# Optimization experiments

Measured on AMD Instinct MI355X. Metric: run time of the kernel, lower is better.

The kernel has to match this reference:

```python
import jax, jax.numpy as jnp
import numpy as np

NUM_EXPS = [8, 16, 64, 256, 1024]
KS = [4, 4, 32, 32, 256]
HIDDEN = 256
OUT_DIM = 3
IN_DIM = 2
N_IMGS = 2
N_COORDS = 1024


def setup_inputs() -> dict:
    key = jax.random.key(0)
    ks = jax.random.split(key, 16)
    inp = {}
    inp["raw_gates"] = jax.random.normal(ks[0], (N_IMGS, sum(NUM_EXPS)), jnp.float32)
    inp["coords"] = jax.random.uniform(ks[1], (N_COORDS, IN_DIM), jnp.float32, -1.0, 1.0)
    fan_in = [IN_DIM] + [HIDDEN] * 4
    fan_out = [HIDDEN * e for e in NUM_EXPS[:-1]] + [OUT_DIM * NUM_EXPS[-1]]
    for i, (fi, fo) in enumerate(zip(fan_in, fan_out)):
        # first_layer_sine_init / sine_init weight scales from the torch module
        bound = (1.0 / fi) if i == 0 else (np.sqrt(6.0 / fi) / 30.0)
        inp[f"W{i}"] = jax.random.uniform(ks[2 + 2 * i], (fo, fi), jnp.float32, -bound, bound)
        bb = 1.0 / np.sqrt(fi)  # torch nn.Linear default bias init
        inp[f"b{i}"] = jax.random.uniform(ks[3 + 2 * i], (fo,), jnp.float32, -bb, bb)
    return inp


def _topk_gate(g, k):
    # torch: topk(|g|, k+1) -> keep top k, gather signed values, scatter into zeros
    _, idx = jax.lax.top_k(jnp.abs(g), min(k + 1, g.shape[1]))
    idx = idx[:, :k]
    vals = jnp.take_along_axis(g, idx, axis=1)
    rows = jnp.arange(g.shape[0])[:, None]
    return jnp.zeros_like(g).at[rows, idx].set(vals)


def _forward(raw_gates, coords, Ws, bs):
    offs = np.cumsum([0] + NUM_EXPS)
    gates = [_topk_gate(raw_gates[:, offs[i]:offs[i + 1]], KS[i]) for i in range(len(NUM_EXPS))]
    Ni = raw_gates.shape[0]
    Nc = coords.shape[0]
    E0 = NUM_EXPS[0]
    # layer 0: shared experts, combine = sparse gates @ expert outputs (== MoECombiner scatter-add)
    h = jnp.sin(30.0 * (coords @ Ws[0].T + bs[0]))            # [Nc, H*E0]
    h = h.reshape(Nc, HIDDEN, E0).transpose(2, 0, 1).reshape(E0, Nc * HIDDEN)  # [E0, Nc*H]
    x = (gates[0] @ h).reshape(Ni, Nc, HIDDEN)                # [Ni, Nc, H]
    for i in range(1, len(NUM_EXPS)):
        E = NUM_EXPS[i]
        h = x @ Ws[i].T + bs[i]                               # [Ni, Nc, d*E]
        if i < len(NUM_EXPS) - 1:
            h = jnp.sin(30.0 * h)
            d = HIDDEN
        else:
            d = OUT_DIM                                       # last layer: no activation
        h = h.reshape(Ni, Nc, d, E)
        x = jnp.einsum('icde,ie->icd', h, gates[i])           # bmm(gate, experts)
    return x


def reference(raw_gates, coords, W0, b0, W1, b1, W2, b2, W3, b3, W4, b4):
    return _forward(raw_gates, coords, (W0, W1, W2, W3, W4), (b0, b1, b2, b3, b4))
```

## Files before the change

### kernel.cpp

```cpp
#include <hip/hip_runtime.h>
#include <math.h>

#define NC 1024
#define HID 256
#define NI 2

typedef _Float16 f16x8 __attribute__((ext_vector_type(8)));
typedef float f32x4 __attribute__((ext_vector_type(4)));
using gvoid = __attribute__((address_space(1))) const void;
using lvoid = __attribute__((address_space(3))) void;

#define LO_SCALE 2048.0f
#define LO_INV (1.0f / 2048.0f)

__global__ __launch_bounds__(1024) void gate_kernel(const float* __restrict__ rg,
                                                    int* __restrict__ gidx,
                                                    float* __restrict__ gval)
{
    const int EDAT[5] = {8, 16, 64, 256, 1024};
    const int KDAT[5] = {4, 4, 32, 32, 256};
    const int OFF[5]  = {0, 8, 24, 88, 344};
    const int level = blockIdx.x, img = blockIdx.y;
    const int E = EDAT[level], K = KDAT[level], off = OFF[level];
    __shared__ float ga[1024];
    const float* src = rg + img * 1368 + off;
    const int t = threadIdx.x;
    if (t < E) ga[t] = src[t];
    __syncthreads();
    if (t < E) {
        const float v = ga[t];
        const float a = fabsf(v);
        int rank = 0;
#pragma unroll 8
        for (int j = 0; j < E; j++) {
            float aj = fabsf(ga[j]);
            rank += (aj > a) || (aj == a && j < t);
        }
        if (rank < K) {
            int base = (level * 2 + img) * 256;
            gidx[base + rank] = t;
            gval[base + rank] = v;
        }
    }
}

__global__ __launch_bounds__(256) void layer0_kernel(const float* __restrict__ coords,
                                                     const float* __restrict__ W0,
                                                     const float* __restrict__ b0,
                                                     const int* __restrict__ gidx,
                                                     const float* __restrict__ gval,
                                                     float* __restrict__ xout)
{
    const int c = blockIdx.x, img = blockIdx.y, h = threadIdx.x;
    __shared__ int gi[4];
    __shared__ float gv[4];
    if (h < 4) {
        int base = (0 * 2 + img) * 256;
        gi[h] = gidx[base + h];
        gv[h] = gval[base + h];
    }
    __syncthreads();
    const float c0 = coords[c * 2], c1 = coords[c * 2 + 1];
    float s = 0.f;
#pragma unroll
    for (int k = 0; k < 4; k++) {
        int row = h * 8 + gi[k];
        s += gv[k] * sinf(30.f * (c0 * W0[row * 2] + c1 * W0[row * 2 + 1] + b0[row]));
    }
    xout[((size_t)img * NC + c) * HID + h] = s;
}

__global__ __launch_bounds__(256) void xpack_kernel(const float* __restrict__ x,
                                                    _Float16* __restrict__ Ap)
{
    const int mt = blockIdx.x, img = blockIdx.y, sa = blockIdx.z;
    const int t = threadIdx.x;
    const int c = t & 63, r0 = t >> 6;
    const float* xb = x + ((size_t)img * NC + mt * 64) * HID;
    _Float16* aph = Ap + ((size_t)(img * 16 + mt) * 8 + sa) * 4096;
    _Float16* apl = aph + 4 * 4096;
    const int kk = sa * 64 + c;
#pragma unroll
    for (int rr = 0; rr < 64; rr += 4) {
        int r = rr + r0;
        float v = xb[r * HID + kk];
        _Float16 h = (_Float16)v;
        int idx = r * 64 + (c ^ ((r & 7) << 3));
        aph[idx] = h;
        apl[idx] = (_Float16)((v - (float)h) * LO_SCALE);
    }
}

__global__ __launch_bounds__(256) void wpack_kernel(const float* __restrict__ W,
                                                    const float* __restrict__ bias,
                                                    const int* __restrict__ gidx,
                                                    const float* __restrict__ gval,
                                                    int level, int E, int lgK,
                                                    _Float16* __restrict__ Bp,
                                                    float* __restrict__ biasP,
                                                    float* __restrict__ gvP,
                                                    int ntiles)
{
    const int ntile = blockIdx.x, img = blockIdx.y, sa = blockIdx.z;
    const int t = threadIdx.x;
    const int N = ntiles * 64;
    __shared__ int wrowS[64];
    const int base = (level * 2 + img) * 256;
    if (t < 64) {
        int n = ntile * 64 + t;
        int dd = n >> lgK, k = n & ((1 << lgK) - 1);
        int wrow = dd * E + gidx[base + k];
        wrowS[t] = wrow;
        if (sa == 0) {
            biasP[img * N + n] = bias[wrow];
            gvP[img * N + n] = gval[base + k];
        }
    }
    __syncthreads();
    const int c = t & 63, r0 = t >> 6;
    const int kk = sa * 64 + c;
    _Float16* bph = Bp + ((size_t)(img * ntiles + ntile) * 8 + sa) * 4096;
    _Float16* bpl = bph + 4 * 4096;
#pragma unroll
    for (int rr = 0; rr < 64; rr += 4) {
        int r = rr + r0;
        float v = W[(size_t)wrowS[r] * HID + kk];
        _Float16 h = (_Float16)v;
        int idx = r * 64 + (c ^ ((r & 7) << 3));
        bph[idx] = h;
        bpl[idx] = (_Float16)((v - (float)h) * LO_SCALE);
    }
}

template <int KGRP, int NNT>
__global__ __launch_bounds__(256) void mid_mfma_kernel(const _Float16* __restrict__ Ap,
                                                       const _Float16* __restrict__ Bp,
                                                       const float* __restrict__ biasP,
                                                       const float* __restrict__ gvP,
                                                       float* __restrict__ x_out)
{
    static_assert(NNT % 8 == 0 || NNT == 8, "NNT multiple of 8");
    constexpr int NNTX = NNT / 8;
    const int b = blockIdx.x;
    const int q = b & 7;
    const int j = b >> 3;
    const int mt = j & 15;
    const int img = (j >> 4) & 1;
    const int nt = q * NNTX + (j >> 5);

    const int tid = threadIdx.x;
    const int wave = tid >> 6, lane = tid & 63;
    const int wm = wave & 1, wn = wave >> 1;
    const int l15 = lane & 15, lhi = lane >> 4;

    __shared__ __align__(16) char lds[49152];
    float* S = (float*)lds;

    const int ntiles = NNT * 2;
    const int N = ntiles * 64;
    const _Float16* ag = Ap + ((size_t)(img * 16 + mt) * 8) * 4096;
    const _Float16* bg = Bp + ((size_t)(img * ntiles + nt * 2) * 8) * 4096;

    auto stage = [&](int off, int ch) {
        const int sa = (ch < 8) ? (ch & 3) : (ch - 4);
        const int sb = (ch < 8) ? ch : (ch - 8);
        const _Float16* gaw = ag + sa * 4096;
#pragma unroll
        for (int q6 = 0; q6 < 6; ++q6) {
            int s = wave * 6 + q6;
            const _Float16* g;
            if (s < 8) {
                g = gaw + s * 512 + lane * 8;
            } else {
                int s8 = s - 8;
                g = bg + ((size_t)((s8 >> 3) * 8 + sb)) * 4096 + (s8 & 7) * 512 + lane * 8;
            }
            __builtin_amdgcn_global_load_lds((gvoid*)g, (lvoid*)(lds + off + s * 1024), 16, 0, 0);
        }
    };

    f32x4 acc[2][4], accL[2][4];
#pragma unroll
    for (int mi = 0; mi < 2; mi++)
#pragma unroll
        for (int ni = 0; ni < 4; ni++) { acc[mi][ni] = (f32x4)0.f; accL[mi][ni] = (f32x4)0.f; }

    stage(0, 0);

    for (int ch = 0; ch < 12; ++ch) {
        const int cur = (ch & 1) * 24576;
        asm volatile("s_waitcnt vmcnt(0)" ::: "memory");
        __syncthreads();
        if (ch < 11) stage(24576 - cur, ch + 1);

        f16x8 af[2][2], bf[2][4];
#pragma unroll
        for (int ks = 0; ks < 2; ++ks) {
#pragma unroll
            for (int mi = 0; mi < 2; ++mi) {
                int row = wm * 32 + mi * 16 + l15;
                int slot = (lhi + 4 * ks) ^ (row & 7);
                af[ks][mi] = *(const f16x8*)(lds + cur + row * 128 + slot * 16);
            }
#pragma unroll
            for (int ni = 0; ni < 4; ++ni) {
                int row = wn * 64 + ni * 16 + l15;
                int slot = (lhi + 4 * ks) ^ (row & 7);
                bf[ks][ni] = *(const f16x8*)(lds + cur + 8192 + row * 128 + slot * 16);
            }
        }
        if (ch < 4) {
#pragma unroll
            for (int ks = 0; ks < 2; ++ks)
#pragma unroll
                for (int mi = 0; mi < 2; ++mi)
#pragma unroll
                    for (int ni = 0; ni < 4; ++ni)
                        acc[mi][ni] = __builtin_amdgcn_mfma_f32_16x16x32_f16(af[ks][mi], bf[ks][ni],
                                                                             acc[mi][ni], 0, 0, 0);
        } else {
#pragma unroll
            for (int ks = 0; ks < 2; ++ks)
#pragma unroll
                for (int mi = 0; mi < 2; ++mi)
#pragma unroll
                    for (int ni = 0; ni < 4; ++ni)
                        accL[mi][ni] = __builtin_amdgcn_mfma_f32_16x16x32_f16(af[ks][mi], bf[ks][ni],
                                                                              accL[mi][ni], 0, 0, 0);
        }
    }
    __syncthreads();

#pragma unroll
    for (int mi = 0; mi < 2; ++mi)
#pragma unroll
        for (int ni = 0; ni < 4; ++ni) {
            int n = wn * 64 + ni * 16 + l15;
            int gn = nt * 128 + n;
            float bv = biasP[img * N + gn];
            float gv = gvP[img * N + gn];
#pragma unroll
            for (int r = 0; r < 4; ++r) {
                int m = wm * 32 + mi * 16 + lhi * 4 + r;
                float val = acc[mi][ni][r] + accL[mi][ni][r] * LO_INV;
                S[m * 129 + n] = gv * sinf(30.f * (val + bv));
            }
        }
    __syncthreads();

    float* xo = x_out + ((size_t)img * NC + mt * 64) * HID;
    if (KGRP == 32) {
        int m = tid >> 2, d = tid & 3;
        float s = 0.f;
#pragma unroll
        for (int jj = 0; jj < 32; ++jj) s += S[m * 129 + d * 32 + ((jj + d * 8) & 31)];
        xo[m * HID + nt * 4 + d] = s;
    } else {
#pragma unroll
        for (int rep = 0; rep < 8; ++rep) {
            int idx = rep * 256 + tid;
            int m = idx >> 5, d = idx & 31;
            const float* Sp = S + m * 129 + d * 4;
            xo[m * HID + nt * 32 + d] = Sp[0] + Sp[1] + Sp[2] + Sp[3];
        }
    }
}

__global__ __launch_bounds__(256) void l4combine_kernel(const float* __restrict__ W4,
                                                        const float* __restrict__ b4,
                                                        const int* __restrict__ gidx,
                                                        const float* __restrict__ gval,
                                                        float* __restrict__ Weff,
                                                        float* __restrict__ beff)
{
    const int d = blockIdx.x, img = blockIdx.y;
    const int t = threadIdx.x;
    const int base = (4 * 2 + img) * 256;
    __shared__ int rows[256];
    __shared__ float gs[256];
    __shared__ float bred[256];
    int e = gidx[base + t];
    float g = gval[base + t];
    rows[t] = (d * 1024 + e) * 256;
    gs[t] = g;
    bred[t] = g * b4[d * 1024 + e];
    __syncthreads();
    float acc = 0.f;
#pragma unroll 4
    for (int k = 0; k < 256; ++k)
        acc = fmaf(gs[k], W4[(size_t)rows[k] + t], acc);
    Weff[(img * 3 + d) * 256 + t] = acc;
    for (int s = 128; s > 0; s >>= 1) {
        if (t < s) bred[t] += bred[t + s];
        __syncthreads();
    }
    if (t == 0) beff[img * 3 + d] = bred[0];
}

__global__ __launch_bounds__(256) void l4apply_kernel(const float* __restrict__ x_in,
                                                      const float* __restrict__ Weff,
                                                      const float* __restrict__ beff,
                                                      float* __restrict__ out)
{
    const int img = blockIdx.y;
    const int c = blockIdx.x * 256 + threadIdx.x;
    __shared__ float ws[3][256];
    __shared__ float bs[3];
    const int t = threadIdx.x;
    if (t < 192) {
        int d = t / 64, k4 = t % 64;
        *(float4*)&ws[d][k4 * 4] = *(const float4*)(Weff + (img * 3 + d) * 256 + k4 * 4);
    }
    if (t < 3) bs[t] = beff[img * 3 + t];
    __syncthreads();
    const float* xb = x_in + ((size_t)img * NC + c) * HID;
    float a0 = 0.f, a1 = 0.f, a2 = 0.f;
#pragma unroll 4
    for (int k = 0; k < 256; k += 4) {
        const float4 xv = *(const float4*)(xb + k);
        const float4 w0 = *(const float4*)&ws[0][k];
        const float4 w1 = *(const float4*)&ws[1][k];
        const float4 w2 = *(const float4*)&ws[2][k];
        a0 += xv.x * w0.x + xv.y * w0.y + xv.z * w0.z + xv.w * w0.w;
        a1 += xv.x * w1.x + xv.y * w1.y + xv.z * w1.z + xv.w * w1.w;
        a2 += xv.x * w2.x + xv.y * w2.y + xv.z * w2.z + xv.w * w2.w;
    }
    float* o = out + ((size_t)img * NC + c) * 3;
    o[0] = a0 + bs[0];
    o[1] = a1 + bs[1];
    o[2] = a2 + bs[2];
}

extern "C" void kernel_launch(void* const* d_in, const int* in_sizes, int n_in,
                              void* d_out, int out_size, void* d_ws, size_t ws_size,
                              hipStream_t stream)
{
    const float* rg     = (const float*)d_in[0];
    const float* coords = (const float*)d_in[1];
    const float* W0 = (const float*)d_in[2];
    const float* b0 = (const float*)d_in[3];
    const float* W1 = (const float*)d_in[4];
    const float* b1 = (const float*)d_in[5];
    const float* W2 = (const float*)d_in[6];
    const float* b2 = (const float*)d_in[7];
    const float* W3 = (const float*)d_in[8];
    const float* b3 = (const float*)d_in[9];
    const float* W4 = (const float*)d_in[10];
    const float* b4 = (const float*)d_in[11];
    float* out = (float*)d_out;

    char* ws = (char*)d_ws;
    int*      gidx  = (int*)ws;
    float*    gval  = (float*)(ws + 10240);
    float*    xA    = (float*)(ws + 20480);
    float*    xB    = (float*)(ws + 2117632);
    _Float16* Ap    = (_Float16*)(ws + 4214784);
    _Float16* Bp    = (_Float16*)(ws + 6311936);
    float*    biasP = (float*)(ws + 23089152);
    float*    gvP   = (float*)(ws + 23154688);
    float*    Weff  = (float*)(ws + 23220224);
    float*    beff  = (float*)(ws + 23228416);

    gate_kernel<<<dim3(5, 2), 1024, 0, stream>>>(rg, gidx, gval);
    l4combine_kernel<<<dim3(3, 2), 256, 0, stream>>>(W4, b4, gidx, gval, Weff, beff);
    layer0_kernel<<<dim3(NC, NI), 256, 0, stream>>>(coords, W0, b0, gidx, gval, xA);

    xpack_kernel<<<dim3(16, 2, 4), 256, 0, stream>>>(xA, Ap);
    wpack_kernel<<<dim3(16, 2, 4), 256, 0, stream>>>(W1, b1, gidx, gval, 1, 16, 2, Bp, biasP, gvP, 16);
    mid_mfma_kernel<4, 8><<<256, 256, 0, stream>>>(Ap, Bp, biasP, gvP, xB);

    xpack_kernel<<<dim3(16, 2, 4), 256, 0, stream>>>(xB, Ap);
    wpack_kernel<<<dim3(128, 2, 4), 256, 0, stream>>>(W2, b2, gidx, gval, 2, 64, 5, Bp, biasP, gvP, 128);
    mid_mfma_kernel<32, 64><<<2048, 256, 0, stream>>>(Ap, Bp, biasP, gvP, xA);

    xpack_kernel<<<dim3(16, 2, 4), 256, 0, stream>>>(xA, Ap);
    wpack_kernel<<<dim3(128, 2, 4), 256, 0, stream>>>(W3, b3, gidx, gval, 3, 256, 5, Bp, biasP, gvP, 128);
    mid_mfma_kernel<32, 64><<<2048, 256, 0, stream>>>(Ap, Bp, biasP, gvP, xB);

    l4apply_kernel<<<dim3(4, 2), 256, 0, stream>>>(xB, Weff, beff, out);
}
```

Measured before the change: 364.8 us.

## Restructure split-fp16 MFMA loop into single-buffered 4-phase staging and use fast sine

The mid-layer MFMA kernel now stages the hi and lo parts of A and B for one K-slice together into a single 48KB LDS buffer. The old loop ran 12 double-buffered chunks with a wait per chunk; the new one runs 4 phases that read fragments into registers, then issue the next stage's loads while the MFMAs run. It also adds a min-blocks-per-CU launch bound of 3 and replaces sinf with __sinf in layer 0 and in the epilogue. The fast sine trades accuracy for speed on arguments scaled by 30, and waiting on one buffer cuts overlap between loading and compute.

```diff
diff --git a/kernel.cpp b/kernel.cpp
--- a/kernel.cpp
+++ b/kernel.cpp
@@ -65,7 +65,7 @@
 #pragma unroll
     for (int k = 0; k < 4; k++) {
         int row = h * 8 + gi[k];
-        s += gv[k] * sinf(30.f * (c0 * W0[row * 2] + c1 * W0[row * 2 + 1] + b0[row]));
+        s += gv[k] * __sinf(30.f * (c0 * W0[row * 2] + c1 * W0[row * 2 + 1] + b0[row]));
     }
     xout[((size_t)img * NC + c) * HID + h] = s;
 }
@@ -133,13 +133,12 @@
 }
 
 template <int KGRP, int NNT>
-__global__ __launch_bounds__(256) void mid_mfma_kernel(const _Float16* __restrict__ Ap,
-                                                       const _Float16* __restrict__ Bp,
-                                                       const float* __restrict__ biasP,
-                                                       const float* __restrict__ gvP,
-                                                       float* __restrict__ x_out)
-{
-    static_assert(NNT % 8 == 0 || NNT == 8, "NNT multiple of 8");
+__global__ __launch_bounds__(256, 3) void mid_mfma_kernel(const _Float16* __restrict__ Ap,
+                                                          const _Float16* __restrict__ Bp,
+                                                          const float* __restrict__ biasP,
+                                                          const float* __restrict__ gvP,
+                                                          float* __restrict__ x_out)
+{
     constexpr int NNTX = NNT / 8;
     const int b = blockIdx.x;
     const int q = b & 7;
@@ -161,21 +160,24 @@
     const _Float16* ag = Ap + ((size_t)(img * 16 + mt) * 8) * 4096;
     const _Float16* bg = Bp + ((size_t)(img * ntiles + nt * 2) * 8) * 4096;
 
-    auto stage = [&](int off, int ch) {
-        const int sa = (ch < 8) ? (ch & 3) : (ch - 4);
-        const int sb = (ch < 8) ? ch : (ch - 8);
-        const _Float16* gaw = ag + sa * 4096;
-#pragma unroll
-        for (int q6 = 0; q6 < 6; ++q6) {
-            int s = wave * 6 + q6;
+    auto stage = [&](int p) {
+        const int s0 = wave * 12;
+#pragma unroll
+        for (int qq = 0; qq < 12; ++qq) {
+            const int s = s0 + qq;
             const _Float16* g;
             if (s < 8) {
-                g = gaw + s * 512 + lane * 8;
+                g = ag + (size_t)p * 4096 + s * 512 + lane * 8;
+            } else if (s < 16) {
+                g = ag + (size_t)(4 + p) * 4096 + (s - 8) * 512 + lane * 8;
+            } else if (s < 32) {
+                int s2 = s - 16;
+                g = bg + (size_t)((s2 >> 3) * 8 + p) * 4096 + (s2 & 7) * 512 + lane * 8;
             } else {
-                int s8 = s - 8;
-                g = bg + ((size_t)((s8 >> 3) * 8 + sb)) * 4096 + (s8 & 7) * 512 + lane * 8;
+                int s2 = s - 32;
+                g = bg + (size_t)((s2 >> 3) * 8 + 4 + p) * 4096 + (s2 & 7) * 512 + lane * 8;
             }
-            __builtin_amdgcn_global_load_lds((gvoid*)g, (lvoid*)(lds + off + s * 1024), 16, 0, 0);
+            __builtin_amdgcn_global_load_lds((gvoid*)g, (lvoid*)(lds + s * 1024), 16, 0, 0);
         }
     };
 
@@ -185,51 +187,60 @@
 #pragma unroll
         for (int ni = 0; ni < 4; ni++) { acc[mi][ni] = (f32x4)0.f; accL[mi][ni] = (f32x4)0.f; }
 
-    stage(0, 0);
-
-    for (int ch = 0; ch < 12; ++ch) {
-        const int cur = (ch & 1) * 24576;
-        asm volatile("s_waitcnt vmcnt(0)" ::: "memory");
-        __syncthreads();
-        if (ch < 11) stage(24576 - cur, ch + 1);
-
-        f16x8 af[2][2], bf[2][4];
-#pragma unroll
-        for (int ks = 0; ks < 2; ++ks) {
+    stage(0);
+    __syncthreads();
+
+#pragma unroll
+    for (int p = 0; p < 4; ++p) {
+        f16x8 afh[2][2], afl[2][2];
+#pragma unroll
+        for (int ks = 0; ks < 2; ++ks)
 #pragma unroll
             for (int mi = 0; mi < 2; ++mi) {
                 int row = wm * 32 + mi * 16 + l15;
-                int slot = (lhi + 4 * ks) ^ (row & 7);
-                af[ks][mi] = *(const f16x8*)(lds + cur + row * 128 + slot * 16);
+                int off = row * 128 + (((lhi + 4 * ks) ^ (row & 7)) * 16);
+                afh[ks][mi] = *(const f16x8*)(lds + off);
+                afl[ks][mi] = *(const f16x8*)(lds + 8192 + off);
             }
+        f16x8 bfh[2][4], bfl[2][4];
+#pragma unroll
+        for (int ks = 0; ks < 2; ++ks)
 #pragma unroll
             for (int ni = 0; ni < 4; ++ni) {
                 int row = wn * 64 + ni * 16 + l15;
-                int slot = (lhi + 4 * ks) ^ (row & 7);
-                bf[ks][ni] = *(const f16x8*)(lds + cur + 8192 + row * 128 + slot * 16);
+                int off = row * 128 + (((lhi + 4 * ks) ^ (row & 7)) * 16);
+                bfh[ks][ni] = *(const f16x8*)(lds + 16384 + off);
+                bfl[ks][ni] = *(const f16x8*)(lds + 32768 + off);
             }
-        }
-        if (ch < 4) {
-#pragma unroll
-            for (int ks = 0; ks < 2; ++ks)
-#pragma unroll
-                for (int mi = 0; mi < 2; ++mi)
-#pragma unroll
-                    for (int ni = 0; ni < 4; ++ni)
-                        acc[mi][ni] = __builtin_amdgcn_mfma_f32_16x16x32_f16(af[ks][mi], bf[ks][ni],
-                                                                             acc[mi][ni], 0, 0, 0);
-        } else {
-#pragma unroll
-            for (int ks = 0; ks < 2; ++ks)
-#pragma unroll
-                for (int mi = 0; mi < 2; ++mi)
-#pragma unroll
-                    for (int ni = 0; ni < 4; ++ni)
-                        accL[mi][ni] = __builtin_amdgcn_mfma_f32_16x16x32_f16(af[ks][mi], bf[ks][ni],
-                                                                              accL[mi][ni], 0, 0, 0);
-        }
-    }
-    __syncthreads();
+        __syncthreads();
+        if (p < 3) stage(p + 1);
+
+#pragma unroll
+        for (int ks = 0; ks < 2; ++ks)
+#pragma unroll
+            for (int mi = 0; mi < 2; ++mi)
+#pragma unroll
+                for (int ni = 0; ni < 4; ++ni)
+                    acc[mi][ni] = __builtin_amdgcn_mfma_f32_16x16x32_f16(afh[ks][mi], bfh[ks][ni],
+                                                                         acc[mi][ni], 0, 0, 0);
+#pragma unroll
+        for (int ks = 0; ks < 2; ++ks)
+#pragma unroll
+            for (int mi = 0; mi < 2; ++mi)
+#pragma unroll
+                for (int ni = 0; ni < 4; ++ni)
+                    accL[mi][ni] = __builtin_amdgcn_mfma_f32_16x16x32_f16(afl[ks][mi], bfh[ks][ni],
+                                                                          accL[mi][ni], 0, 0, 0);
+#pragma unroll
+        for (int ks = 0; ks < 2; ++ks)
+#pragma unroll
+            for (int mi = 0; mi < 2; ++mi)
+#pragma unroll
+                for (int ni = 0; ni < 4; ++ni)
+                    accL[mi][ni] = __builtin_amdgcn_mfma_f32_16x16x32_f16(afh[ks][mi], bfl[ks][ni],
+                                                                          accL[mi][ni], 0, 0, 0);
+        __syncthreads();
+    }
 
 #pragma unroll
     for (int mi = 0; mi < 2; ++mi)
@@ -243,7 +254,7 @@
             for (int r = 0; r < 4; ++r) {
                 int m = wm * 32 + mi * 16 + lhi * 4 + r;
                 float val = acc[mi][ni][r] + accL[mi][ni][r] * LO_INV;
-                S[m * 129 + n] = gv * sinf(30.f * (val + bv));
+                S[m * 129 + n] = gv * __sinf(30.f * (val + bv));
             }
         }
     __syncthreads();
```

New measurement: 540.4 us. +48.1%, slower.

## Enlarge MFMA tile to 128x128 and restructure split-f16 staging and sin

Applied to the files above, without the earlier changes.

The mid-layer MFMA kernel now computes a 128x128 output tile per block instead of 64x128, which halves the grid and doubles per-block reuse of the B tiles. Each pipeline stage loads hi and lo planes for A and B together, 64KB per buffer and 128KB double-buffered. The three hi/lo product terms (hi*hi, lo*hi, hi*lo) are issued in one loop instead of separate chunk phases. Precise sinf is replaced by the fast __sinf intrinsic in layer0 and the epilogue. This adds accuracy risk, since arguments reach about 30 in magnitude, and the 128KB LDS with launch bounds of 1 limits occupancy to one block per CU.

```diff
diff --git a/kernel.cpp b/kernel.cpp
--- a/kernel.cpp
+++ b/kernel.cpp
@@ -65,7 +65,7 @@
 #pragma unroll
     for (int k = 0; k < 4; k++) {
         int row = h * 8 + gi[k];
-        s += gv[k] * sinf(30.f * (c0 * W0[row * 2] + c1 * W0[row * 2 + 1] + b0[row]));
+        s += gv[k] * __sinf(30.f * (c0 * W0[row * 2] + c1 * W0[row * 2 + 1] + b0[row]));
     }
     xout[((size_t)img * NC + c) * HID + h] = s;
 }
@@ -132,107 +132,105 @@
     }
 }
 
-template <int KGRP, int NNT>
-__global__ __launch_bounds__(256) void mid_mfma_kernel(const _Float16* __restrict__ Ap,
-                                                       const _Float16* __restrict__ Bp,
-                                                       const float* __restrict__ biasP,
-                                                       const float* __restrict__ gvP,
-                                                       float* __restrict__ x_out)
-{
-    static_assert(NNT % 8 == 0 || NNT == 8, "NNT multiple of 8");
-    constexpr int NNTX = NNT / 8;
+template <int KGRP, int NTB>
+__global__ __launch_bounds__(256, 1) void mid_mfma_kernel(const _Float16* __restrict__ Ap,
+                                                          const _Float16* __restrict__ Bp,
+                                                          const float* __restrict__ biasP,
+                                                          const float* __restrict__ gvP,
+                                                          float* __restrict__ x_out)
+{
+    constexpr int NTBX = NTB / 8;
     const int b = blockIdx.x;
     const int q = b & 7;
     const int j = b >> 3;
-    const int mt = j & 15;
-    const int img = (j >> 4) & 1;
-    const int nt = q * NNTX + (j >> 5);
+    const int mtp = j & 7;
+    const int img = (j >> 3) & 1;
+    const int ntl = j >> 4;
+    const int nt = q * NTBX + ntl;
 
     const int tid = threadIdx.x;
     const int wave = tid >> 6, lane = tid & 63;
     const int wm = wave & 1, wn = wave >> 1;
     const int l15 = lane & 15, lhi = lane >> 4;
 
-    __shared__ __align__(16) char lds[49152];
+    __shared__ __align__(16) char lds[131072];
     float* S = (float*)lds;
 
-    const int ntiles = NNT * 2;
-    const int N = ntiles * 64;
-    const _Float16* ag = Ap + ((size_t)(img * 16 + mt) * 8) * 4096;
+    const int ntiles = NTB * 2;
+    const int N = NTB * 128;
+    const _Float16* ag = Ap + ((size_t)(img * 16 + mtp * 2) * 8) * 4096;
     const _Float16* bg = Bp + ((size_t)(img * ntiles + nt * 2) * 8) * 4096;
 
-    auto stage = [&](int off, int ch) {
-        const int sa = (ch < 8) ? (ch & 3) : (ch - 4);
-        const int sb = (ch < 8) ? ch : (ch - 8);
-        const _Float16* gaw = ag + sa * 4096;
-#pragma unroll
-        for (int q6 = 0; q6 < 6; ++q6) {
-            int s = wave * 6 + q6;
-            const _Float16* g;
-            if (s < 8) {
-                g = gaw + s * 512 + lane * 8;
-            } else {
-                int s8 = s - 8;
-                g = bg + ((size_t)((s8 >> 3) * 8 + sb)) * 4096 + (s8 & 7) * 512 + lane * 8;
-            }
-            __builtin_amdgcn_global_load_lds((gvoid*)g, (lvoid*)(lds + off + s * 1024), 16, 0, 0);
+    const _Float16* sbase = (wave & 2) ? bg : ag;
+    const int planeAdd = (wave & 1) ? 4 : 0;
+    auto stage = [&](int bufoff, int p) {
+#pragma unroll
+        for (int qq = 0; qq < 16; ++qq) {
+            const _Float16* g = sbase + (size_t)(qq >> 3) * 32768
+                              + (planeAdd + p) * 4096 + (qq & 7) * 512 + lane * 8;
+            __builtin_amdgcn_global_load_lds((gvoid*)g,
+                (lvoid*)(lds + bufoff + wave * 16384 + qq * 1024), 16, 0, 0);
         }
     };
 
-    f32x4 acc[2][4], accL[2][4];
-#pragma unroll
-    for (int mi = 0; mi < 2; mi++)
+    f32x4 acc[4][4], accL[4][4];
+#pragma unroll
+    for (int mi = 0; mi < 4; mi++)
 #pragma unroll
         for (int ni = 0; ni < 4; ni++) { acc[mi][ni] = (f32x4)0.f; accL[mi][ni] = (f32x4)0.f; }
 
     stage(0, 0);
 
-    for (int ch = 0; ch < 12; ++ch) {
-        const int cur = (ch & 1) * 24576;
+#pragma unroll
+    for (int p = 0; p < 4; ++p) {
+        const int cur = (p & 1) * 65536;
         asm volatile("s_waitcnt vmcnt(0)" ::: "memory");
         __syncthreads();
-        if (ch < 11) stage(24576 - cur, ch + 1);
-
-        f16x8 af[2][2], bf[2][4];
+        if (p < 3) stage(65536 - cur, p + 1);
+
 #pragma unroll
         for (int ks = 0; ks < 2; ++ks) {
-#pragma unroll
-            for (int mi = 0; mi < 2; ++mi) {
-                int row = wm * 32 + mi * 16 + l15;
-                int slot = (lhi + 4 * ks) ^ (row & 7);
-                af[ks][mi] = *(const f16x8*)(lds + cur + row * 128 + slot * 16);
+            f16x8 ah[4], al[4], bh[4], bl[4];
+#pragma unroll
+            for (int mi = 0; mi < 4; ++mi) {
+                int row = wm * 64 + mi * 16 + l15;
+                int off = (row >> 6) * 8192 + (row & 63) * 128
+                        + (((lhi + 4 * ks) ^ (row & 7)) * 16);
+                ah[mi] = *(const f16x8*)(lds + cur + off);
+                al[mi] = *(const f16x8*)(lds + cur + 16384 + off);
             }
 #pragma unroll
             for (int ni = 0; ni < 4; ++ni) {
                 int row = wn * 64 + ni * 16 + l15;
-                int slot = (lhi + 4 * ks) ^ (row & 7);
-                bf[ks][ni] = *(const f16x8*)(lds + cur + 8192 + row * 128 + slot * 16);
+                int off = (row >> 6) * 8192 + (row & 63) * 128
+                        + (((lhi + 4 * ks) ^ (row & 7)) * 16);
+                bh[ni] = *(const f16x8*)(lds + cur + 32768 + off);
+                bl[ni] = *(const f16x8*)(lds + cur + 49152 + off);
             }
-        }
-        if (ch < 4) {
-#pragma unroll
-            for (int ks = 0; ks < 2; ++ks)
-#pragma unroll
-                for (int mi = 0; mi < 2; ++mi)
-#pragma unroll
-                    for (int ni = 0; ni < 4; ++ni)
-                        acc[mi][ni] = __builtin_amdgcn_mfma_f32_16x16x32_f16(af[ks][mi], bf[ks][ni],
-                                                                             acc[mi][ni], 0, 0, 0);
-        } else {
-#pragma unroll
-            for (int ks = 0; ks < 2; ++ks)
-#pragma unroll
-                for (int mi = 0; mi < 2; ++mi)
-#pragma unroll
-                    for (int ni = 0; ni < 4; ++ni)
-                        accL[mi][ni] = __builtin_amdgcn_mfma_f32_16x16x32_f16(af[ks][mi], bf[ks][ni],
-                                                                              accL[mi][ni], 0, 0, 0);
-        }
-    }
-    __syncthreads();
-
-#pragma unroll
-    for (int mi = 0; mi < 2; ++mi)
+#pragma unroll
+            for (int mi = 0; mi < 4; ++mi)
+#pragma unroll
+                for (int ni = 0; ni < 4; ++ni)
+                    acc[mi][ni] = __builtin_amdgcn_mfma_f32_16x16x32_f16(ah[mi], bh[ni],
+                                                                         acc[mi][ni], 0, 0, 0);
+#pragma unroll
+            for (int mi = 0; mi < 4; ++mi)
+#pragma unroll
+                for (int ni = 0; ni < 4; ++ni)
+                    accL[mi][ni] = __builtin_amdgcn_mfma_f32_16x16x32_f16(al[mi], bh[ni],
+                                                                          accL[mi][ni], 0, 0, 0);
+#pragma unroll
+            for (int mi = 0; mi < 4; ++mi)
+#pragma unroll
+                for (int ni = 0; ni < 4; ++ni)
+                    accL[mi][ni] = __builtin_amdgcn_mfma_f32_16x16x32_f16(ah[mi], bl[ni],
+                                                                          accL[mi][ni], 0, 0, 0);
+        }
+    }
+    __syncthreads();
+
+#pragma unroll
+    for (int mi = 0; mi < 4; ++mi)
 #pragma unroll
         for (int ni = 0; ni < 4; ++ni) {
             int n = wn * 64 + ni * 16 + l15;
@@ -241,27 +239,31 @@
             float gv = gvP[img * N + gn];
 #pragma unroll
             for (int r = 0; r < 4; ++r) {
-                int m = wm * 32 + mi * 16 + lhi * 4 + r;
+                int m = wm * 64 + mi * 16 + lhi * 4 + r;
                 float val = acc[mi][ni][r] + accL[mi][ni][r] * LO_INV;
-                S[m * 129 + n] = gv * sinf(30.f * (val + bv));
+                S[m * 129 + n] = gv * __sinf(30.f * (val + bv));
             }
         }
     __syncthreads();
 
-    float* xo = x_out + ((size_t)img * NC + mt * 64) * HID;
+    float* xo = x_out + ((size_t)img * NC + mtp * 128) * HID;
     if (KGRP == 32) {
-        int m = tid >> 2, d = tid & 3;
-        float s = 0.f;
-#pragma unroll
-        for (int jj = 0; jj < 32; ++jj) s += S[m * 129 + d * 32 + ((jj + d * 8) & 31)];
-        xo[m * HID + nt * 4 + d] = s;
+#pragma unroll
+        for (int rep = 0; rep < 2; ++rep) {
+            int idx = rep * 256 + tid;
+            int m = idx >> 2, d = idx & 3;
+            float s = 0.f;
+#pragma unroll
+            for (int jj = 0; jj < 32; ++jj) s += S[m * 129 + d * 32 + ((jj + d * 8) & 31)];
+            xo[m * HID + nt * 4 + d] = s;
+        }
     } else {
 #pragma unroll
-        for (int rep = 0; rep < 8; ++rep) {
+        for (int rep = 0; rep < 16; ++rep) {
             int idx = rep * 256 + tid;
-            int m = idx >> 5, d = idx & 31;
-            const float* Sp = S + m * 129 + d * 4;
-            xo[m * HID + nt * 32 + d] = Sp[0] + Sp[1] + Sp[2] + Sp[3];
+            int m = idx >> 5, dl = idx & 31;
+            const float* Sp = S + m * 129 + dl * 4;
+            xo[m * HID + nt * 32 + dl] = Sp[0] + Sp[1] + Sp[2] + Sp[3];
         }
     }
 }
@@ -367,15 +369,15 @@
 
     xpack_kernel<<<dim3(16, 2, 4), 256, 0, stream>>>(xA, Ap);
     wpack_kernel<<<dim3(16, 2, 4), 256, 0, stream>>>(W1, b1, gidx, gval, 1, 16, 2, Bp, biasP, gvP, 16);
-    mid_mfma_kernel<4, 8><<<256, 256, 0, stream>>>(Ap, Bp, biasP, gvP, xB);
+    mid_mfma_kernel<4, 8><<<128, 256, 0, stream>>>(Ap, Bp, biasP, gvP, xB);
 
     xpack_kernel<<<dim3(16, 2, 4), 256, 0, stream>>>(xB, Ap);
     wpack_kernel<<<dim3(128, 2, 4), 256, 0, stream>>>(W2, b2, gidx, gval, 2, 64, 5, Bp, biasP, gvP, 128);
-    mid_mfma_kernel<32, 64><<<2048, 256, 0, stream>>>(Ap, Bp, biasP, gvP, xA);
+    mid_mfma_kernel<32, 64><<<1024, 256, 0, stream>>>(Ap, Bp, biasP, gvP, xA);
 
     xpack_kernel<<<dim3(16, 2, 4), 256, 0, stream>>>(xA, Ap);
     wpack_kernel<<<dim3(128, 2, 4), 256, 0, stream>>>(W3, b3, gidx, gval, 3, 256, 5, Bp, biasP, gvP, 128);
-    mid_mfma_kernel<32, 64><<<2048, 256, 0, stream>>>(Ap, Bp, biasP, gvP, xB);
+    mid_mfma_kernel<32, 64><<<1024, 256, 0, stream>>>(Ap, Bp, biasP, gvP, xB);
 
     l4apply_kernel<<<dim3(4, 2), 256, 0, stream>>>(xB, Weff, beff, out);
 }
```

After: 312.7 us. 1.17x faster.
